# Optimization experiments

Measured on AMD Instinct MI355X. Metric: run time of the kernel, lower is better.

The kernel has to match this reference:

```python
import jax, jax.numpy as jnp
import numpy as np

NX, NY, C = 784, 480, 32
N0 = NX * NY          # 376320 level-0 nodes
N1 = N0 // 4          # 94080
N2 = N0 // 16         # 23520


def _gcn(x, w, b, ei, n):
    """PyG GCNConv: add self loops, symmetric norm, linear, scatter-sum, bias."""
    loop = jnp.arange(n, dtype=ei.dtype)
    src = jnp.concatenate([ei[0], loop])
    dst = jnp.concatenate([ei[1], loop])
    deg = jax.ops.segment_sum(jnp.ones(src.shape[0], x.dtype), dst, num_segments=n)
    dinv = jnp.where(deg > 0, jax.lax.rsqrt(deg), 0.0)
    norm = (dinv[src] * dinv[dst])[:, None]          # [E+n, 1]
    msg = (x @ w)[src] * norm                        # gather + scale
    return jax.ops.segment_sum(msg, dst, num_segments=n) + b


def _up2(x, h, w):
    """2x nearest-neighbor upsample of a row-major-flattened (h, w, C) grid."""
    g = x.reshape(h, w, x.shape[-1])
    return jnp.repeat(jnp.repeat(g, 2, axis=0), 2, axis=1).reshape(-1, x.shape[-1])


def setup_inputs() -> dict:
    key = jax.random.key(0)
    ks = jax.random.split(key, 20)
    f32 = jnp.float32
    inp = {
        "x": jax.random.normal(ks[0], (N0, 4), f32),
        "fc1_w": jax.random.normal(ks[1], (4, C), f32) * 0.1,
        "fc1_b": jax.random.normal(ks[2], (C,), f32) * 0.1,
        "w1": jax.random.normal(ks[3], (C, C), f32) * 0.1,
        "b1": jax.random.normal(ks[4], (C,), f32) * 0.1,
        "w2": jax.random.normal(ks[5], (C, C), f32) * 0.1,
        "b2": jax.random.normal(ks[6], (C,), f32) * 0.1,
        "w3": jax.random.normal(ks[7], (C, C), f32) * 0.1,
        "b3": jax.random.normal(ks[8], (C,), f32) * 0.1,
        "w4": jax.random.normal(ks[9], (C, C), f32) * 0.1,
        "b4": jax.random.normal(ks[10], (C,), f32) * 0.1,
        "w5": jax.random.normal(ks[11], (C, C), f32) * 0.1,
        "b5": jax.random.normal(ks[12], (C,), f32) * 0.1,
        "fc2_w": jax.random.normal(ks[13], (C, 3), f32) * 0.1,
        "fc2_b": jax.random.normal(ks[14], (3,), f32) * 0.1,
        "idx0": jnp.arange(N0, dtype=jnp.int32),
        "idx1": jnp.arange(N1, dtype=jnp.int32),
        "idx2": jnp.arange(N2, dtype=jnp.int32),
        "ei0": jax.random.randint(ks[15], (2, 4 * N0), 0, N0, dtype=jnp.int32),
        "ei1": jax.random.randint(ks[16], (2, 4 * N1), 0, N1, dtype=jnp.int32),
        "ei2": jax.random.randint(ks[17], (2, 4 * N2), 0, N2, dtype=jnp.int32),
    }
    return inp


def reference(x, fc1_w, fc1_b, w1, b1, w2, b2, w3, b3, w4, b4, w5, b5,
              fc2_w, fc2_b, idx0, idx1, idx2, ei0, ei1, ei2):
    h = jax.nn.relu(x @ fc1_w + fc1_b)                                  # [N0, 32]
    h = h.at[idx0].set(_gcn(h[idx0], w1, b1, ei0, idx0.shape[0]))
    h = jax.nn.relu(h)
    # level-1 downsample: take every other grid row/col
    h1 = h.reshape(NX, NY, C)[::2, ::2].reshape(-1, C)                  # [N1, 32]
    h1 = h1.at[idx1].set(_gcn(h1[idx1], w2, b2, ei1, idx1.shape[0]))
    h1 = jax.nn.relu(h1)
    # level-2 downsample
    h2 = h1.reshape(NX // 2, NY // 2, C)[::2, ::2].reshape(-1, C)       # [N2, 32]
    h2 = h2.at[idx2].set(_gcn(h2[idx2], w3, b3, ei2, idx2.shape[0]))
    h2 = jax.nn.relu(h2)
    # upsample level-2 -> level-1, residual add
    h1u = h1 + _up2(h2, NX // 4, NY // 4)
    h1u = h1u.at[idx1].set(_gcn(h1u[idx1], w4, b4, ei1, idx1.shape[0]))
    h1u = jax.nn.relu(h1u)
    # upsample level-1 -> level-0, residual add
    hu = h + _up2(h1u, NX // 2, NY // 2)
    hu = hu.at[idx0].set(_gcn(hu[idx0], w5, b5, ei0, idx0.shape[0]))
    hu = jax.nn.relu(hu)
    return (hu @ fc2_w + fc2_b)[idx0]                                   # [N0, 3]
```

## Files before the change

### kernel.cpp

```cpp
#include <hip/hip_runtime.h>
#include <hip/hip_bf16.h>

typedef unsigned short u16;
typedef unsigned int u32;
typedef float fx2 __attribute__((ext_vector_type(2)));

#define NXg 784
#define NYg 480
constexpr int N0c = NXg * NYg;
constexpr int N1c = N0c / 4;
constexpr int N2c = N0c / 16;
constexpr int NTc = N0c + N1c + N2c;
constexpr int E0c = 4 * N0c;
constexpr int E1c = 4 * N1c;
constexpr int E2c = 4 * N2c;
constexpr int Etot = E0c + E1c + E2c;
constexpr int P0c = E0c + 3 * N0c;
constexpr int P1c = E1c + 3 * N1c;
constexpr int P2c = E2c + 3 * N2c;
constexpr int Ptot = P0c + P1c + P2c;
constexpr int NB0 = (N0c + 1023) / 1024;
constexpr int NB1 = (N1c + 1023) / 1024;
constexpr int NB2 = (N2c + 1023) / 1024;
constexpr int NBt = NB0 + NB1 + NB2;

__device__ __forceinline__ float bf2f(u16 v) {
    union { u32 u; float f; } t; t.u = ((u32)v) << 16; return t.f;
}
__device__ __forceinline__ u16 f2bf(float f) {
    union { float f; u32 u; } t; t.f = f;
    u32 u = t.u;
    u32 r = (u + 0x7fffu + ((u >> 16) & 1u)) >> 16;
    return (u16)r;
}
__device__ __forceinline__ float rdf(const void* p, int i, int isf32) {
    if (isf32) return ((const float*)p)[i];
    return bf2f(((const u16*)p)[i]);
}
__device__ __forceinline__ void stage(float* dst, const void* src, int n, int isf32) {
    int t = threadIdx.x;
    if (isf32) {
        const float* s = (const float*)src;
        for (int i = t; i < n; i += 256) dst[i] = s[i];
    } else {
        const u16* s = (const u16*)src;
        for (int i = t; i < n; i += 256) dst[i] = bf2f(s[i]);
    }
}

struct F32S {
    typedef float T;
    static __device__ __forceinline__ float ld(const T* p, size_t i) { return p[i]; }
    static __device__ __forceinline__ void st(T* p, size_t i, float v) { p[i] = v; }
    static __device__ __forceinline__ fx2 ld2(const T* p, size_t i) {
        return ((const fx2*)p)[i];
    }
    static __device__ __forceinline__ void st2nt(T* p, size_t i, fx2 v) {
        __builtin_nontemporal_store(v, (fx2*)p + i);
    }
};
struct BF16S {
    typedef u16 T;
    static __device__ __forceinline__ float ld(const T* p, size_t i) { return bf2f(p[i]); }
    static __device__ __forceinline__ void st(T* p, size_t i, float v) { p[i] = f2bf(v); }
    static __device__ __forceinline__ fx2 ld2(const T* p, size_t i) {
        u32 w = ((const u32*)p)[i];
        fx2 r; r.x = bf2f((u16)(w & 0xffffu)); r.y = bf2f((u16)(w >> 16));
        return r;
    }
    static __device__ __forceinline__ void st2nt(T* p, size_t i, fx2 v) {
        u32 w = (u32)f2bf(v.x) | ((u32)f2bf(v.y) << 16);
        __builtin_nontemporal_store(w, (u32*)p + i);
    }
};

__device__ __forceinline__ void lvl_of_bin(int b, int& lv, int& bl) {
    if (b < NB0) { lv = 0; bl = b; }
    else if (b < NB0 + NB1) { lv = 1; bl = b - NB0; }
    else { lv = 2; bl = b - NB0 - NB1; }
}

__global__ void k_dinit(const u32* __restrict__ xw, int* __restrict__ flag,
                        int* __restrict__ binCnt, u16* __restrict__ y0,
                        u16* __restrict__ y1, u16* __restrict__ y2) {
    __shared__ int cnt;
    int t = threadIdx.x;
    int g = blockIdx.x * 256 + t;
    if (blockIdx.x == 0) {
        if (t == 0) cnt = 0;
        __syncthreads();
        u32 w = xw[t];
        int e = (int)((w >> 7) & 0xFFu);
        int hit = ((e >= 90 && e <= 135) || ((w & 0x7FFFu) == 0u)) ? 1 : 0;
        atomicAdd(&cnt, hit);
        __syncthreads();
        if (t == 0) *flag = (cnt < 192) ? 1 : 0;
    }
    if (g < NBt) binCnt[g] = 0;
    if (blockIdx.x == 1 && t < 32) { y0[t] = 0; y1[t] = 0; y2[t] = 0; }
}

__global__ void kA_count(const int* __restrict__ ei0, const int* __restrict__ ei1,
                         const int* __restrict__ ei2, int* __restrict__ binCnt) {
    __shared__ int lc[NB0];
    int b = blockIdx.x, t = threadIdx.x;
    int lv, bl; lvl_of_bin(b, lv, bl);
    const int* dstp; int E, nb, binB;
    if (lv == 0) { dstp = ei0 + E0c; E = E0c; nb = NB0; binB = 0; }
    else if (lv == 1) { dstp = ei1 + E1c; E = E1c; nb = NB1; binB = NB0; }
    else { dstp = ei2 + E2c; E = E2c; nb = NB2; binB = NB0 + NB1; }
    for (int i = t; i < nb; i += 256) lc[i] = 0;
    __syncthreads();
    int e0 = bl * 4096, e1 = min(E, e0 + 4096);
    for (int i = e0 + t; i < e1; i += 256) atomicAdd(&lc[dstp[i] >> 10], 1);
    __syncthreads();
    for (int i = t; i < nb; i += 256) if (lc[i]) atomicAdd(&binCnt[binB + i], lc[i]);
}

__global__ void kB_scan(const int* __restrict__ binCnt, int* __restrict__ binStart,
                        int* __restrict__ binCursor) {
    __shared__ int s[512];
    int t = threadIdx.x;
    int v = (t < NBt) ? binCnt[t] : 0;
    s[t] = v;
    __syncthreads();
    for (int off = 1; off < 512; off <<= 1) {
        int x = (t >= off) ? s[t - off] : 0;
        __syncthreads();
        s[t] += x;
        __syncthreads();
    }
    if (t < NBt) { int e = s[t] - v; binStart[t] = e; binCursor[t] = e; }
    if (t == 0) binStart[NBt] = Etot;
}

__global__ void kC_place(const int* __restrict__ ei0, const int* __restrict__ ei1,
                         const int* __restrict__ ei2, int* __restrict__ binCursor,
                         u32* __restrict__ BE) {
    __shared__ int lc[NB0];
    __shared__ int lb[NB0];
    int b = blockIdx.x, t = threadIdx.x;
    int lv, bl; lvl_of_bin(b, lv, bl);
    const int* srcp; const int* dstp; int E, nb, binB;
    if (lv == 0) { srcp = ei0; dstp = ei0 + E0c; E = E0c; nb = NB0; binB = 0; }
    else if (lv == 1) { srcp = ei1; dstp = ei1 + E1c; E = E1c; nb = NB1; binB = NB0; }
    else { srcp = ei2; dstp = ei2 + E2c; E = E2c; nb = NB2; binB = NB0 + NB1; }
    for (int i = t; i < nb; i += 256) lc[i] = 0;
    __syncthreads();
    int e0 = bl * 4096, e1 = min(E, e0 + 4096);
    for (int i = e0 + t; i < e1; i += 256) atomicAdd(&lc[dstp[i] >> 10], 1);
    __syncthreads();
    for (int i = t; i < nb; i += 256) {
        int c = lc[i];
        lb[i] = c ? atomicAdd(&binCursor[binB + i], c) : 0;
        lc[i] = 0;
    }
    __syncthreads();
    for (int i = e0 + t; i < e1; i += 256) {
        int d = dstp[i];
        int bn = d >> 10;
        int p = atomicAdd(&lc[bn], 1);
        BE[lb[bn] + p] = ((u32)srcp[i] << 10) | (u32)(d & 1023);
    }
}

__global__ void kD1_count(const u32* __restrict__ BE, const int* __restrict__ binStart,
                          int* __restrict__ CNT, float* __restrict__ DINV,
                          int* __restrict__ binPadTot) {
    __shared__ int lc[1024];
    __shared__ int red[256];
    int b = blockIdx.x, t = threadIdx.x;
    int lv, bl; lvl_of_bin(b, lv, bl);
    int cbase, nLev;
    if (lv == 0) { cbase = 0; nLev = N0c; }
    else if (lv == 1) { cbase = N0c; nLev = N1c; }
    else { cbase = N0c + N1c; nLev = N2c; }
    for (int i = t; i < 1024; i += 256) lc[i] = 0;
    __syncthreads();
    int s0 = binStart[b], s1 = binStart[b + 1];
    for (int i = s0 + t; i < s1; i += 256) {
        atomicAdd(&lc[BE[i] & 1023u], 1);
    }
    __syncthreads();
    int nodeB = bl << 10;
    int ps = 0;
#pragma unroll
    for (int j = 0; j < 4; j++) {
        int li = t * 4 + j;
        int node = nodeB + li;
        if (node < nLev) {
            int c = lc[li];
            CNT[cbase + node] = c;
            DINV[cbase + node] = rsqrtf((float)c + 1.0f);
            ps += (c + 3) & ~3;
        }
    }
    red[t] = ps;
    __syncthreads();
    for (int off = 128; off > 0; off >>= 1) {
        if (t < off) red[t] += red[t + off];
        __syncthreads();
    }
    if (t == 0) binPadTot[b] = red[0];
}

__global__ void kD2_scan(const int* __restrict__ binPadTot, int* __restrict__ binPadStart) {
    __shared__ int s[512];
    __shared__ int tot0, tot01;
    int t = threadIdx.x;
    int v = (t < NBt) ? binPadTot[t] : 0;
    s[t] = v;
    __syncthreads();
    for (int off = 1; off < 512; off <<= 1) {
        int x = (t >= off) ? s[t - off] : 0;
        __syncthreads();
        s[t] += x;
        __syncthreads();
    }
    if (t == 0) { tot0 = s[NB0 - 1]; tot01 = s[NB0 + NB1 - 1]; }
    __syncthreads();
    if (t < NBt) {
        int ex = s[t] - v;
        int cb, sub;
        if (t < NB0) { cb = 0; sub = 0; }
        else if (t < NB0 + NB1) { cb = P0c; sub = tot0; }
        else { cb = P0c + P1c; sub = tot01; }
        binPadStart[t] = cb + ex - sub;
    }
}

__global__ void kD3_final(const u32* __restrict__ BE, const int* __restrict__ binStart,
                          const int* __restrict__ CNT, const int* __restrict__ binPadStart,
                          int* __restrict__ rowptr, int* __restrict__ colAll) {
    __shared__ int lst[1024];
    __shared__ int lcur[1024];
    __shared__ int red[256];
    int b = blockIdx.x, t = threadIdx.x;
    int lv, bl; lvl_of_bin(b, lv, bl);
    int cbase, nLev, dummy;
    if (lv == 0) { cbase = 0; nLev = N0c; dummy = N0c; }
    else if (lv == 1) { cbase = N0c; nLev = N1c; dummy = N1c; }
    else { cbase = N0c + N1c; nLev = N2c; dummy = N2c; }
    int nodeB = bl << 10;
    int pc[4];
    int ps = 0;
#pragma unroll
    for (int j = 0; j < 4; j++) {
        int li = t * 4 + j;
        int node = nodeB + li;
        int c = (node < nLev) ? CNT[cbase + node] : 0;
        pc[j] = (c + 3) & ~3;
        ps += pc[j];
    }
    red[t] = ps;
    __syncthreads();
    for (int off = 1; off < 256; off <<= 1) {
        int x = (t >= off) ? red[t - off] : 0;
        __syncthreads();
        red[t] += x;
        __syncthreads();
    }
    int ex = red[t] - ps;
    int tot = red[255];
    int off = ex;
#pragma unroll
    for (int j = 0; j < 4; j++) {
        int li = t * 4 + j;
        lst[li] = off;
        lcur[li] = off;
        off += pc[j];
    }
    int cb = binPadStart[b];
#pragma unroll
    for (int j = 0; j < 4; j++) {
        int li = t * 4 + j;
        int node = nodeB + li;
        if (node < nLev) rowptr[cbase + node] = cb + lst[li];
    }
    __syncthreads();
    for (int i = t; i < tot; i += 256) colAll[cb + i] = dummy;
    __syncthreads();
    int s0 = binStart[b], s1 = binStart[b + 1];
    for (int i = s0 + t; i < s1; i += 256) {
        u32 e = BE[i];
        int p = atomicAdd(&lcur[e & 1023u], 1);
        colAll[cb + p] = (int)(e >> 10);
    }
}

template <class SIn>
__device__ __forceinline__ fx2 gather2(const typename SIn::T* __restrict__ ys,
                                       const int* __restrict__ rp,
                                       const int* __restrict__ cnt,
                                       const int* __restrict__ col,
                                       const float* __restrict__ dinv,
                                       int node, int cp) {
    int s0 = rp[node];
    int nch = (cnt[node] + 3) >> 2;
    fx2 a = SIn::ld2(ys, (size_t)node * 16 + cp);
    const int4* c4 = (const int4*)(col + s0);
    for (int i = 0; i < nch; i++) {
        int4 cs = c4[i];
        fx2 a0 = SIn::ld2(ys, (size_t)cs.x * 16 + cp);
        fx2 a1 = SIn::ld2(ys, (size_t)cs.y * 16 + cp);
        fx2 a2 = SIn::ld2(ys, (size_t)cs.z * 16 + cp);
        fx2 a3 = SIn::ld2(ys, (size_t)cs.w * 16 + cp);
        a += (a0 + a1) + (a2 + a3);
    }
    float di = dinv[node];
    a *= di;
    return a;
}

constexpr int FC1_TILES = N0c / 64;
__global__ void k_fc1prep(const void* __restrict__ x, const void* __restrict__ fw,
                          const void* __restrict__ fb, const void* __restrict__ w1,
                          const float* __restrict__ d0, u16* __restrict__ ys1,
                          const int* __restrict__ flag) {
    int isf32 = *flag;
    __shared__ float sx[256];
    __shared__ float sh[64 * 33];
    __shared__ float sfw[128];
    __shared__ float sfb[32];
    __shared__ float sw1[1024];
    int t = threadIdx.x;
    stage(sw1, w1, 1024, isf32);
    stage(sfw, fw, 128, isf32);
    stage(sfb, fb, 32, isf32);
    __syncthreads();
    int c = t & 31;
    int ng = t >> 5;
    int ci0 = t & 15;
    int rgrp = t >> 4;
    for (int tile = blockIdx.x; tile < FC1_TILES; tile += gridDim.x) {
        int nodeBase = tile * 64;
        sx[t] = rdf(x, nodeBase * 4 + t, isf32);
        __syncthreads();
#pragma unroll
        for (int i = 0; i < 8; i++) {
            int ln = ng + i * 8;
            float a = sfb[c];
#pragma unroll
            for (int k = 0; k < 4; k++) a = fmaf(sx[ln * 4 + k], sfw[k * 32 + c], a);
            sh[ln * 33 + c] = fmaxf(a, 0.0f);
        }
        __syncthreads();
        float acc[4][2];
#pragma unroll
        for (int r = 0; r < 4; r++) { acc[r][0] = 0.0f; acc[r][1] = 0.0f; }
#pragma unroll
        for (int k = 0; k < 32; k++) {
            float w0 = sw1[k * 32 + ci0];
            float w1v = sw1[k * 32 + ci0 + 16];
#pragma unroll
            for (int r = 0; r < 4; r++) {
                float s = sh[(rgrp * 4 + r) * 33 + k];
                acc[r][0] = fmaf(s, w0, acc[r][0]);
                acc[r][1] = fmaf(s, w1v, acc[r][1]);
            }
        }
#pragma unroll
        for (int r = 0; r < 4; r++) {
            int node = nodeBase + rgrp * 4 + r;
            float dv = d0[node];
            BF16S::st(ys1, (size_t)node * 32 + ci0, acc[r][0] * dv);
            BF16S::st(ys1, (size_t)node * 32 + ci0 + 16, acc[r][1] * dv);
        }
        __syncthreads();
    }
}

template <class SIn, class SRes, class SOut, int NPB>
__global__ void k_gds(const typename SIn::T* __restrict__ ys_in, const int* __restrict__ rp,
                      const int* __restrict__ cnt, const int* __restrict__ col,
                      const float* __restrict__ dinv_p, const void* __restrict__ b,
                      typename SRes::T* __restrict__ O, const void* __restrict__ wn,
                      const float* __restrict__ dinv_c, typename SOut::T* __restrict__ ys_out,
                      int cols, const int* __restrict__ flag) {
    int isf32 = *flag;
    __shared__ float sv[NPB * 32];
    __shared__ float swn[1024];
    int t = threadIdx.x;
    int nodeBase = blockIdx.x * NPB;
    int rb = nodeBase / cols;
    if (!(rb & 1)) stage(swn, wn, 1024, isf32);
    int cp = t & 15;
#pragma unroll
    for (int i = 0; i < NPB / 16; i++) {
        int local = (t >> 4) + i * 16;
        int node = nodeBase + local;
        fx2 g = gather2<SIn>(ys_in, rp, cnt, col, dinv_p, node, cp);
        fx2 v;
        v.x = fmaxf(g.x + rdf(b, 2 * cp, isf32), 0.0f);
        v.y = fmaxf(g.y + rdf(b, 2 * cp + 1, isf32), 0.0f);
        SRes::st2nt(O, (size_t)node * 16 + cp, v);
        sv[local * 32 + 2 * cp] = v.x;
        sv[local * 32 + 2 * cp + 1] = v.y;
    }
    __syncthreads();
    if (!(rb & 1)) {
#pragma unroll
        for (int i = 0; i < NPB / 16; i++) {
            int item = t + i * 256;
            int childIdx = item >> 5;
            int ci = item & 31;
            int lc = childIdx * 2;
            int cc = (nodeBase - rb * cols) + lc;
            int dn = (rb >> 1) * (cols >> 1) + (cc >> 1);
            float a = 0.0f;
#pragma unroll
            for (int k = 0; k < 32; k++) a = fmaf(sv[lc * 32 + k], swn[k * 32 + ci], a);
            SOut::st(ys_out, (size_t)dn * 32 + ci, a * dinv_c[dn]);
        }
    }
}

template <class SIn, class SRes, class SOut, int NPB>
__global__ void k_gup(const typename SIn::T* __restrict__ ys_in, const int* __restrict__ rp,
                      const int* __restrict__ cnt, const int* __restrict__ col,
                      const float* __restrict__ dinv_p, const void* __restrict__ b,
                      const typename SRes::T* __restrict__ R, const void* __restrict__ wn,
                      const float* __restrict__ dinv_c, typename SOut::T* __restrict__ ys_out,
                      int cols_p, const int* __restrict__ flag) {
    constexpr int RPT = NPB / 4;
    int isf32 = *flag;
    __shared__ float sv[NPB * 32];
    __shared__ float sch[NPB * 4 * 33];
    __shared__ float swn[1024];
    int t = threadIdx.x;
    int nodeBase = blockIdx.x * NPB;
    stage(swn, wn, 1024, isf32);
    if (t < NPB * 16) {
        int local = t >> 4, cp = t & 15;
        int node = nodeBase + local;
        fx2 g = gather2<SIn>(ys_in, rp, cnt, col, dinv_p, node, cp);
        sv[local * 32 + 2 * cp] = fmaxf(g.x + rdf(b, 2 * cp, isf32), 0.0f);
        sv[local * 32 + 2 * cp + 1] = fmaxf(g.y + rdf(b, 2 * cp + 1, isf32), 0.0f);
    }
    __syncthreads();
    int rb = nodeBase / cols_p;
    int ccb = nodeBase - rb * cols_p;
    int cols_c = cols_p * 2;
#pragma unroll
    for (int i = 0; i < NPB / 2; i++) {
        int item = t + i * 256;
        int row = item >> 5, k = item & 31;
        int lp = row >> 2, j = row & 3;
        int ch = (2 * rb + (j >> 1)) * cols_c + 2 * (ccb + lp) + (j & 1);
        sch[row * 33 + k] = SRes::ld(R, (size_t)ch * 32 + k) + sv[lp * 32 + k];
    }
    __syncthreads();
    int ci0 = t & 15;
    int rgrp = t >> 4;
    float acc[RPT][2];
#pragma unroll
    for (int r = 0; r < RPT; r++) { acc[r][0] = 0.0f; acc[r][1] = 0.0f; }
#pragma unroll
    for (int k = 0; k < 32; k++) {
        float w0 = swn[k * 32 + ci0];
        float w1v = swn[k * 32 + ci0 + 16];
#pragma unroll
        for (int r = 0; r < RPT; r++) {
            float s = sch[(rgrp * RPT + r) * 33 + k];
            acc[r][0] = fmaf(s, w0, acc[r][0]);
            acc[r][1] = fmaf(s, w1v, acc[r][1]);
        }
    }
#pragma unroll
    for (int r = 0; r < RPT; r++) {
        int row = rgrp * RPT + r;
        int lp = row >> 2, j = row & 3;
        int ch = (2 * rb + (j >> 1)) * cols_c + 2 * (ccb + lp) + (j & 1);
        float dc = dinv_c[ch];
        SOut::st(ys_out, (size_t)ch * 32 + ci0, acc[r][0] * dc);
        SOut::st(ys_out, (size_t)ch * 32 + ci0 + 16, acc[r][1] * dc);
    }
}

__global__ void k_gfc2(const u16* __restrict__ ys, const int* __restrict__ rp,
                       const int* __restrict__ cnt, const int* __restrict__ col,
                       const float* __restrict__ dinv, const void* __restrict__ b5,
                       const void* __restrict__ fw, const void* __restrict__ fb,
                       void* __restrict__ out, int n, const int* __restrict__ flag) {
    int isf32 = *flag;
    __shared__ float sv[1024];
    __shared__ float sw[96];
    __shared__ float sfb[3];
    int t = threadIdx.x;
    if (t < 96) sw[t] = rdf(fw, t, isf32);
    if (t < 3) sfb[t] = rdf(fb, t, isf32);
    int nodeBase = blockIdx.x * 32;
    int cp = t & 15;
#pragma unroll
    for (int i = 0; i < 2; i++) {
        int local = (t >> 4) + i * 16;
        int node = nodeBase + local;
        fx2 g = gather2<BF16S>(ys, rp, cnt, col, dinv, node, cp);
        sv[local * 32 + 2 * cp] = fmaxf(g.x + rdf(b5, 2 * cp, isf32), 0.0f);
        sv[local * 32 + 2 * cp + 1] = fmaxf(g.y + rdf(b5, 2 * cp + 1, isf32), 0.0f);
    }
    __syncthreads();
    if (t < 96) {
        int ln = t / 3, j = t - ln * 3;
        int gn = nodeBase + ln;
        float o = sfb[j];
#pragma unroll
        for (int k = 0; k < 32; k++) o = fmaf(sv[ln * 32 + k], sw[k * 3 + j], o);
        if (isf32) ((float*)out)[(size_t)gn * 3 + j] = o;
        else ((u16*)out)[(size_t)gn * 3 + j] = f2bf(o);
    }
}

extern "C" void kernel_launch(void* const* d_in, const int* in_sizes, int n_in,
                              void* d_out, int out_size, void* d_ws, size_t ws_size,
                              hipStream_t stream) {
    const void* x    = d_in[0];
    const void* fc1w = d_in[1];
    const void* fc1b = d_in[2];
    const void* w1 = d_in[3];  const void* b1 = d_in[4];
    const void* w2 = d_in[5];  const void* b2 = d_in[6];
    const void* w3 = d_in[7];  const void* b3 = d_in[8];
    const void* w4 = d_in[9];  const void* b4 = d_in[10];
    const void* w5 = d_in[11]; const void* b5 = d_in[12];
    const void* fc2w = d_in[13]; const void* fc2b = d_in[14];
    const int* ei0 = (const int*)d_in[18];
    const int* ei1 = (const int*)d_in[19];
    const int* ei2 = (const int*)d_in[20];

    u16* YS0 = (u16*)d_ws;
    u16* A   = YS0 + (size_t)(N0c + 1) * 32;
    u16* YS1 = A + (size_t)N0c * 32;
    u16* H1  = YS1 + (size_t)(N1c + 1) * 32;
    u16* YS2 = H1 + (size_t)N1c * 32;
    float* DINV = (float*)(YS2 + (size_t)(N2c + 1) * 32);
    int* CNT   = (int*)(DINV + NTc);
    int* RPA   = CNT + NTc;
    int* COLA  = RPA + NTc;
    u32* BE    = (u32*)(COLA + Ptot);
    int* binCnt      = (int*)(BE + Etot);
    int* binStart    = binCnt + NBt;
    int* binCursor   = binStart + NBt + 1;
    int* binPadTot   = binCursor + NBt;
    int* binPadStart = binPadTot + NBt;
    int* FLAG        = binPadStart + NBt;

    float* D0 = DINV; float* D1 = D0 + N0c; float* D2 = D1 + N1c;
    int* C0 = CNT;  int* C1 = C0 + N0c;  int* C2 = C1 + N1c;
    int* RP0 = RPA; int* RP1 = RP0 + N0c; int* RP2 = RP1 + N1c;

    const int Bk = 256;

    k_dinit<<<2, Bk, 0, stream>>>((const u32*)x, FLAG, binCnt,
                                  YS0 + (size_t)N0c * 32, YS1 + (size_t)N1c * 32,
                                  YS2 + (size_t)N2c * 32);

    kA_count<<<NBt, Bk, 0, stream>>>(ei0, ei1, ei2, binCnt);
    kB_scan<<<1, 512, 0, stream>>>(binCnt, binStart, binCursor);
    kC_place<<<NBt, Bk, 0, stream>>>(ei0, ei1, ei2, binCursor, BE);
    kD1_count<<<NBt, Bk, 0, stream>>>(BE, binStart, CNT, DINV, binPadTot);
    kD2_scan<<<1, 512, 0, stream>>>(binPadTot, binPadStart);
    kD3_final<<<NBt, Bk, 0, stream>>>(BE, binStart, CNT, binPadStart, RPA, COLA);

    k_fc1prep<<<1960, Bk, 0, stream>>>(x, fc1w, fc1b, w1, D0, YS0, FLAG);
    k_gds<BF16S, BF16S, BF16S, 32><<<N0c / 32, Bk, 0, stream>>>(YS0, RP0, C0, COLA, D0, b1, A, w2, D1, YS1, NYg, FLAG);
    k_gds<BF16S, BF16S, BF16S, 16><<<N1c / 16, Bk, 0, stream>>>(YS1, RP1, C1, COLA, D1, b2, H1, w3, D2, YS2, NYg / 2, FLAG);
    k_gup<BF16S, BF16S, BF16S, 8><<<N2c / 8, Bk, 0, stream>>>(YS2, RP2, C2, COLA, D2, b3, H1, w4, D1, YS1, NYg / 4, FLAG);
    k_gup<BF16S, BF16S, BF16S, 16><<<N1c / 16, Bk, 0, stream>>>(YS1, RP1, C1, COLA, D1, b4, A, w5, D0, YS0, NYg / 2, FLAG);
    k_gfc2<<<N0c / 32, Bk, 0, stream>>>(YS0, RP0, C0, COLA, D0, b5, fc2w, fc2b, d_out, N0c, FLAG);
}
```

Before: 351.4 us.

## Fuse CSR build into one kernel and pack rowptr with chunk count

```diff
diff --git a/kernel.cpp b/kernel.cpp
--- a/kernel.cpp
+++ b/kernel.cpp
@@ -15,14 +15,11 @@
 constexpr int E1c = 4 * N1c;
 constexpr int E2c = 4 * N2c;
 constexpr int Etot = E0c + E1c + E2c;
-constexpr int P0c = E0c + 3 * N0c;
-constexpr int P1c = E1c + 3 * N1c;
-constexpr int P2c = E2c + 3 * N2c;
-constexpr int Ptot = P0c + P1c + P2c;
 constexpr int NB0 = (N0c + 1023) / 1024;
 constexpr int NB1 = (N1c + 1023) / 1024;
 constexpr int NB2 = (N2c + 1023) / 1024;
 constexpr int NBt = NB0 + NB1 + NB2;
+constexpr int COLcap = Etot + 3076 * NBt + 16;
 
 __device__ __forceinline__ float bf2f(u16 v) {
     union { u32 u; float f; } t; t.u = ((u32)v) << 16; return t.f;
@@ -48,17 +45,6 @@
     }
 }
 
-struct F32S {
-    typedef float T;
-    static __device__ __forceinline__ float ld(const T* p, size_t i) { return p[i]; }
-    static __device__ __forceinline__ void st(T* p, size_t i, float v) { p[i] = v; }
-    static __device__ __forceinline__ fx2 ld2(const T* p, size_t i) {
-        return ((const fx2*)p)[i];
-    }
-    static __device__ __forceinline__ void st2nt(T* p, size_t i, fx2 v) {
-        __builtin_nontemporal_store(v, (fx2*)p + i);
-    }
-};
 struct BF16S {
     typedef u16 T;
     static __device__ __forceinline__ float ld(const T* p, size_t i) { return bf2f(p[i]); }
@@ -164,74 +150,10 @@
     }
 }
 
-__global__ void kD1_count(const u32* __restrict__ BE, const int* __restrict__ binStart,
-                          int* __restrict__ CNT, float* __restrict__ DINV,
-                          int* __restrict__ binPadTot) {
+__global__ void kD_all(const u32* __restrict__ BE, const int* __restrict__ binStart,
+                       float* __restrict__ DINV, u32* __restrict__ RPC,
+                       int* __restrict__ colAll) {
     __shared__ int lc[1024];
-    __shared__ int red[256];
-    int b = blockIdx.x, t = threadIdx.x;
-    int lv, bl; lvl_of_bin(b, lv, bl);
-    int cbase, nLev;
-    if (lv == 0) { cbase = 0; nLev = N0c; }
-    else if (lv == 1) { cbase = N0c; nLev = N1c; }
-    else { cbase = N0c + N1c; nLev = N2c; }
-    for (int i = t; i < 1024; i += 256) lc[i] = 0;
-    __syncthreads();
-    int s0 = binStart[b], s1 = binStart[b + 1];
-    for (int i = s0 + t; i < s1; i += 256) {
-        atomicAdd(&lc[BE[i] & 1023u], 1);
-    }
-    __syncthreads();
-    int nodeB = bl << 10;
-    int ps = 0;
-#pragma unroll
-    for (int j = 0; j < 4; j++) {
-        int li = t * 4 + j;
-        int node = nodeB + li;
-        if (node < nLev) {
-            int c = lc[li];
-            CNT[cbase + node] = c;
-            DINV[cbase + node] = rsqrtf((float)c + 1.0f);
-            ps += (c + 3) & ~3;
-        }
-    }
-    red[t] = ps;
-    __syncthreads();
-    for (int off = 128; off > 0; off >>= 1) {
-        if (t < off) red[t] += red[t + off];
-        __syncthreads();
-    }
-    if (t == 0) binPadTot[b] = red[0];
-}
-
-__global__ void kD2_scan(const int* __restrict__ binPadTot, int* __restrict__ binPadStart) {
-    __shared__ int s[512];
-    __shared__ int tot0, tot01;
-    int t = threadIdx.x;
-    int v = (t < NBt) ? binPadTot[t] : 0;
-    s[t] = v;
-    __syncthreads();
-    for (int off = 1; off < 512; off <<= 1) {
-        int x = (t >= off) ? s[t - off] : 0;
-        __syncthreads();
-        s[t] += x;
-        __syncthreads();
-    }
-    if (t == 0) { tot0 = s[NB0 - 1]; tot01 = s[NB0 + NB1 - 1]; }
-    __syncthreads();
-    if (t < NBt) {
-        int ex = s[t] - v;
-        int cb, sub;
-        if (t < NB0) { cb = 0; sub = 0; }
-        else if (t < NB0 + NB1) { cb = P0c; sub = tot0; }
-        else { cb = P0c + P1c; sub = tot01; }
-        binPadStart[t] = cb + ex - sub;
-    }
-}
-
-__global__ void kD3_final(const u32* __restrict__ BE, const int* __restrict__ binStart,
-                          const int* __restrict__ CNT, const int* __restrict__ binPadStart,
-                          int* __restrict__ rowptr, int* __restrict__ colAll) {
     __shared__ int lst[1024];
     __shared__ int lcur[1024];
     __shared__ int red[256];
@@ -241,6 +163,11 @@
     if (lv == 0) { cbase = 0; nLev = N0c; dummy = N0c; }
     else if (lv == 1) { cbase = N0c; nLev = N1c; dummy = N1c; }
     else { cbase = N0c + N1c; nLev = N2c; dummy = N2c; }
+    for (int i = t; i < 1024; i += 256) lc[i] = 0;
+    __syncthreads();
+    int s0 = binStart[b], s1 = binStart[b + 1];
+    for (int i = s0 + t; i < s1; i += 256) atomicAdd(&lc[BE[i] & 1023u], 1);
+    __syncthreads();
     int nodeB = bl << 10;
     int pc[4];
     int ps = 0;
@@ -248,7 +175,7 @@
     for (int j = 0; j < 4; j++) {
         int li = t * 4 + j;
         int node = nodeB + li;
-        int c = (node < nLev) ? CNT[cbase + node] : 0;
+        int c = (node < nLev) ? lc[li] : 0;
         pc[j] = (c + 3) & ~3;
         ps += pc[j];
     }
@@ -262,6 +189,7 @@
     }
     int ex = red[t] - ps;
     int tot = red[255];
+    int cb = (s0 & ~3) + 3076 * b;
     int off = ex;
 #pragma unroll
     for (int j = 0; j < 4; j++) {
@@ -270,17 +198,21 @@
         lcur[li] = off;
         off += pc[j];
     }
-    int cb = binPadStart[b];
+    __syncthreads();
 #pragma unroll
     for (int j = 0; j < 4; j++) {
         int li = t * 4 + j;
         int node = nodeB + li;
-        if (node < nLev) rowptr[cbase + node] = cb + lst[li];
-    }
-    __syncthreads();
+        if (node < nLev) {
+            int c = lc[li];
+            DINV[cbase + node] = rsqrtf((float)c + 1.0f);
+            int rp = cb + lst[li];
+            u32 nch = (u32)((c + 3) >> 2);
+            RPC[cbase + node] = ((u32)(rp >> 2) << 10) | nch;
+        }
+    }
     for (int i = t; i < tot; i += 256) colAll[cb + i] = dummy;
     __syncthreads();
-    int s0 = binStart[b], s1 = binStart[b + 1];
     for (int i = s0 + t; i < s1; i += 256) {
         u32 e = BE[i];
         int p = atomicAdd(&lcur[e & 1023u], 1);
@@ -288,23 +220,22 @@
     }
 }
 
-template <class SIn>
-__device__ __forceinline__ fx2 gather2(const typename SIn::T* __restrict__ ys,
-                                       const int* __restrict__ rp,
-                                       const int* __restrict__ cnt,
+__device__ __forceinline__ fx2 gather2(const u16* __restrict__ ys,
+                                       const u32* __restrict__ rpc,
                                        const int* __restrict__ col,
                                        const float* __restrict__ dinv,
                                        int node, int cp) {
-    int s0 = rp[node];
-    int nch = (cnt[node] + 3) >> 2;
-    fx2 a = SIn::ld2(ys, (size_t)node * 16 + cp);
+    u32 v = rpc[node];
+    int s0 = (int)((v >> 10) << 2);
+    int nch = (int)(v & 1023u);
+    fx2 a = BF16S::ld2(ys, (size_t)node * 16 + cp);
     const int4* c4 = (const int4*)(col + s0);
     for (int i = 0; i < nch; i++) {
         int4 cs = c4[i];
-        fx2 a0 = SIn::ld2(ys, (size_t)cs.x * 16 + cp);
-        fx2 a1 = SIn::ld2(ys, (size_t)cs.y * 16 + cp);
-        fx2 a2 = SIn::ld2(ys, (size_t)cs.z * 16 + cp);
-        fx2 a3 = SIn::ld2(ys, (size_t)cs.w * 16 + cp);
+        fx2 a0 = BF16S::ld2(ys, (size_t)cs.x * 16 + cp);
+        fx2 a1 = BF16S::ld2(ys, (size_t)cs.y * 16 + cp);
+        fx2 a2 = BF16S::ld2(ys, (size_t)cs.z * 16 + cp);
+        fx2 a3 = BF16S::ld2(ys, (size_t)cs.w * 16 + cp);
         a += (a0 + a1) + (a2 + a3);
     }
     float di = dinv[node];
@@ -370,12 +301,12 @@
     }
 }
 
-template <class SIn, class SRes, class SOut, int NPB>
-__global__ void k_gds(const typename SIn::T* __restrict__ ys_in, const int* __restrict__ rp,
-                      const int* __restrict__ cnt, const int* __restrict__ col,
+template <int NPB>
+__global__ void k_gds(const u16* __restrict__ ys_in, const u32* __restrict__ rpc,
+                      const int* __restrict__ col,
                       const float* __restrict__ dinv_p, const void* __restrict__ b,
-                      typename SRes::T* __restrict__ O, const void* __restrict__ wn,
-                      const float* __restrict__ dinv_c, typename SOut::T* __restrict__ ys_out,
+                      u16* __restrict__ O, const void* __restrict__ wn,
+                      const float* __restrict__ dinv_c, u16* __restrict__ ys_out,
                       int cols, const int* __restrict__ flag) {
     int isf32 = *flag;
     __shared__ float sv[NPB * 32];
@@ -389,11 +320,11 @@
     for (int i = 0; i < NPB / 16; i++) {
         int local = (t >> 4) + i * 16;
         int node = nodeBase + local;
-        fx2 g = gather2<SIn>(ys_in, rp, cnt, col, dinv_p, node, cp);
+        fx2 g = gather2(ys_in, rpc, col, dinv_p, node, cp);
         fx2 v;
         v.x = fmaxf(g.x + rdf(b, 2 * cp, isf32), 0.0f);
         v.y = fmaxf(g.y + rdf(b, 2 * cp + 1, isf32), 0.0f);
-        SRes::st2nt(O, (size_t)node * 16 + cp, v);
+        BF16S::st2nt(O, (size_t)node * 16 + cp, v);
         sv[local * 32 + 2 * cp] = v.x;
         sv[local * 32 + 2 * cp + 1] = v.y;
     }
@@ -410,17 +341,17 @@
             float a = 0.0f;
 #pragma unroll
             for (int k = 0; k < 32; k++) a = fmaf(sv[lc * 32 + k], swn[k * 32 + ci], a);
-            SOut::st(ys_out, (size_t)dn * 32 + ci, a * dinv_c[dn]);
-        }
-    }
-}
-
-template <class SIn, class SRes, class SOut, int NPB>
-__global__ void k_gup(const typename SIn::T* __restrict__ ys_in, const int* __restrict__ rp,
-                      const int* __restrict__ cnt, const int* __restrict__ col,
+            BF16S::st(ys_out, (size_t)dn * 32 + ci, a * dinv_c[dn]);
+        }
+    }
+}
+
+template <int NPB>
+__global__ void k_gup(const u16* __restrict__ ys_in, const u32* __restrict__ rpc,
+                      const int* __restrict__ col,
                       const float* __restrict__ dinv_p, const void* __restrict__ b,
-                      const typename SRes::T* __restrict__ R, const void* __restrict__ wn,
-                      const float* __restrict__ dinv_c, typename SOut::T* __restrict__ ys_out,
+                      const u16* __restrict__ R, const void* __restrict__ wn,
+                      const float* __restrict__ dinv_c, u16* __restrict__ ys_out,
                       int cols_p, const int* __restrict__ flag) {
     constexpr int RPT = NPB / 4;
     int isf32 = *flag;
@@ -433,7 +364,7 @@
     if (t < NPB * 16) {
         int local = t >> 4, cp = t & 15;
         int node = nodeBase + local;
-        fx2 g = gather2<SIn>(ys_in, rp, cnt, col, dinv_p, node, cp);
+        fx2 g = gather2(ys_in, rpc, col, dinv_p, node, cp);
         sv[local * 32 + 2 * cp] = fmaxf(g.x + rdf(b, 2 * cp, isf32), 0.0f);
         sv[local * 32 + 2 * cp + 1] = fmaxf(g.y + rdf(b, 2 * cp + 1, isf32), 0.0f);
     }
@@ -447,7 +378,7 @@
         int row = item >> 5, k = item & 31;
         int lp = row >> 2, j = row & 3;
         int ch = (2 * rb + (j >> 1)) * cols_c + 2 * (ccb + lp) + (j & 1);
-        sch[row * 33 + k] = SRes::ld(R, (size_t)ch * 32 + k) + sv[lp * 32 + k];
+        sch[row * 33 + k] = bf2f(R[(size_t)ch * 32 + k]) + sv[lp * 32 + k];
     }
     __syncthreads();
     int ci0 = t & 15;
@@ -472,13 +403,13 @@
         int lp = row >> 2, j = row & 3;
         int ch = (2 * rb + (j >> 1)) * cols_c + 2 * (ccb + lp) + (j & 1);
         float dc = dinv_c[ch];
-        SOut::st(ys_out, (size_t)ch * 32 + ci0, acc[r][0] * dc);
-        SOut::st(ys_out, (size_t)ch * 32 + ci0 + 16, acc[r][1] * dc);
-    }
-}
-
-__global__ void k_gfc2(const u16* __restrict__ ys, const int* __restrict__ rp,
-                       const int* __restrict__ cnt, const int* __restrict__ col,
+        BF16S::st(ys_out, (size_t)ch * 32 + ci0, acc[r][0] * dc);
+        BF16S::st(ys_out, (size_t)ch * 32 + ci0 + 16, acc[r][1] * dc);
+    }
+}
+
+__global__ void k_gfc2(const u16* __restrict__ ys, const u32* __restrict__ rpc,
+                       const int* __restrict__ col,
                        const float* __restrict__ dinv, const void* __restrict__ b5,
                        const void* __restrict__ fw, const void* __restrict__ fb,
                        void* __restrict__ out, int n, const int* __restrict__ flag) {
@@ -495,7 +426,7 @@
     for (int i = 0; i < 2; i++) {
         int local = (t >> 4) + i * 16;
         int node = nodeBase + local;
-        fx2 g = gather2<BF16S>(ys, rp, cnt, col, dinv, node, cp);
+        fx2 g = gather2(ys, rpc, col, dinv, node, cp);
         sv[local * 32 + 2 * cp] = fmaxf(g.x + rdf(b5, 2 * cp, isf32), 0.0f);
         sv[local * 32 + 2 * cp + 1] = fmaxf(g.y + rdf(b5, 2 * cp + 1, isf32), 0.0f);
     }
@@ -533,20 +464,16 @@
     u16* H1  = YS1 + (size_t)(N1c + 1) * 32;
     u16* YS2 = H1 + (size_t)N1c * 32;
     float* DINV = (float*)(YS2 + (size_t)(N2c + 1) * 32);
-    int* CNT   = (int*)(DINV + NTc);
-    int* RPA   = CNT + NTc;
-    int* COLA  = RPA + NTc;
-    u32* BE    = (u32*)(COLA + Ptot);
-    int* binCnt      = (int*)(BE + Etot);
-    int* binStart    = binCnt + NBt;
-    int* binCursor   = binStart + NBt + 1;
-    int* binPadTot   = binCursor + NBt;
-    int* binPadStart = binPadTot + NBt;
-    int* FLAG        = binPadStart + NBt;
+    u32* RPC  = (u32*)(DINV + NTc);
+    int* COLA = (int*)(RPC + NTc);
+    u32* BE   = (u32*)(COLA + COLcap);
+    int* binCnt    = (int*)(BE + Etot);
+    int* binStart  = binCnt + NBt;
+    int* binCursor = binStart + NBt + 1;
+    int* FLAG      = binCursor + NBt;
 
     float* D0 = DINV; float* D1 = D0 + N0c; float* D2 = D1 + N1c;
-    int* C0 = CNT;  int* C1 = C0 + N0c;  int* C2 = C1 + N1c;
-    int* RP0 = RPA; int* RP1 = RP0 + N0c; int* RP2 = RP1 + N1c;
+    u32* RPC0 = RPC; u32* RPC1 = RPC0 + N0c; u32* RPC2 = RPC1 + N1c;
 
     const int Bk = 256;
 
@@ -557,14 +484,12 @@
     kA_count<<<NBt, Bk, 0, stream>>>(ei0, ei1, ei2, binCnt);
     kB_scan<<<1, 512, 0, stream>>>(binCnt, binStart, binCursor);
     kC_place<<<NBt, Bk, 0, stream>>>(ei0, ei1, ei2, binCursor, BE);
-    kD1_count<<<NBt, Bk, 0, stream>>>(BE, binStart, CNT, DINV, binPadTot);
-    kD2_scan<<<1, 512, 0, stream>>>(binPadTot, binPadStart);
-    kD3_final<<<NBt, Bk, 0, stream>>>(BE, binStart, CNT, binPadStart, RPA, COLA);
+    kD_all<<<NBt, Bk, 0, stream>>>(BE, binStart, DINV, RPC, COLA);
 
     k_fc1prep<<<1960, Bk, 0, stream>>>(x, fc1w, fc1b, w1, D0, YS0, FLAG);
-    k_gds<BF16S, BF16S, BF16S, 32><<<N0c / 32, Bk, 0, stream>>>(YS0, RP0, C0, COLA, D0, b1, A, w2, D1, YS1, NYg, FLAG);
-    k_gds<BF16S, BF16S, BF16S, 16><<<N1c / 16, Bk, 0, stream>>>(YS1, RP1, C1, COLA, D1, b2, H1, w3, D2, YS2, NYg / 2, FLAG);
-    k_gup<BF16S, BF16S, BF16S, 8><<<N2c / 8, Bk, 0, stream>>>(YS2, RP2, C2, COLA, D2, b3, H1, w4, D1, YS1, NYg / 4, FLAG);
-    k_gup<BF16S, BF16S, BF16S, 16><<<N1c / 16, Bk, 0, stream>>>(YS1, RP1, C1, COLA, D1, b4, A, w5, D0, YS0, NYg / 2, FLAG);
-    k_gfc2<<<N0c / 32, Bk, 0, stream>>>(YS0, RP0, C0, COLA, D0, b5, fc2w, fc2b, d_out, N0c, FLAG);
-}
+    k_gds<32><<<N0c / 32, Bk, 0, stream>>>(YS0, RPC0, COLA, D0, b1, A, w2, D1, YS1, NYg, FLAG);
+    k_gds<16><<<N1c / 16, Bk, 0, stream>>>(YS1, RPC1, COLA, D1, b2, H1, w3, D2, YS2, NYg / 2, FLAG);
+    k_gup<8><<<N2c / 8, Bk, 0, stream>>>(YS2, RPC2, COLA, D2, b3, H1, w4, D1, YS1, NYg / 4, FLAG);
+    k_gup<16><<<N1c / 16, Bk, 0, stream>>>(YS1, RPC1, COLA, D1, b4, A, w5, D0, YS0, NYg / 2, FLAG);
+    k_gfc2<<<N0c / 32, Bk, 0, stream>>>(YS0, RPC0, COLA, D0, b5, fc2w, fc2b, d_out, N0c, FLAG);
+}
```

Result: faster. 337.8 us (-3.8%).
